# Performance work log

Hardware: AMD Instinct MI355X
Metric: run time of the kernel (lower is better)

The kernel has to match this reference:

```python
import jax, jax.numpy as jnp
import numpy as np

NUM_HEADS = 16
EPS = 1e-6
ROPE_BASE = 10000.0

def _thw(N, TT):
    table = {2640: (3, 22, 40), 1530: (3, 17, 30), 6120: (3, 34, 60), 660: (3, 11, 20)}
    return table.get(N - TT, (3, 23, 40))

def _positions(t, h, w):
    tt, hh, ww = np.meshgrid(np.arange(t), np.arange(h), np.arange(w), indexing='ij')
    return jnp.asarray(np.stack([tt, hh, ww], -1).reshape(-1, 3), jnp.float32)  # (THW, 3)

def _rope1d(x, pos):
    # x: (B,H,T,d) one axis-chunk, pos: (T,) positions for that axis
    d = x.shape[-1]
    inv_freq = 1.0 / (ROPE_BASE ** (jnp.arange(0, d, 2, dtype=jnp.float32) / d))
    ang = pos[:, None] * inv_freq                     # (T, d/2)
    cos = jnp.concatenate([jnp.cos(ang)] * 2, -1)     # (T, d)
    sin = jnp.concatenate([jnp.sin(ang)] * 2, -1)
    x1, x2 = x[..., : d // 2], x[..., d // 2:]
    return x * cos + jnp.concatenate([-x2, x1], -1) * sin

def _rope3d(x, pos, TT):
    # first TT tokens (text) pass through; video tokens get per-axis rotation
    pre, vid = x[:, :, :TT], x[:, :, TT:]
    chunks = jnp.split(vid, 3, axis=-1)               # t/h/w axis chunks
    rot = [_rope1d(c, pos[:, i]) for i, c in enumerate(chunks)]
    return jnp.concatenate([pre, jnp.concatenate(rot, -1)], axis=2)

def _rms(x, w):
    return x * jax.lax.rsqrt(jnp.mean(x * x, -1, keepdims=True) + EPS) * w

def setup_inputs() -> dict:
    key = jax.random.key(0)
    ks = jax.random.split(key, 12)
    B, N, C = 1, 2866, 1536
    Dh = C // NUM_HEADS
    s = 0.02
    return {
        'x': jax.random.normal(ks[0], (B, N, C), jnp.float32),
        'Wq': jax.random.normal(ks[1], (C, C), jnp.float32) * s,
        'bq': jnp.zeros((C,), jnp.float32),
        'Wk': jax.random.normal(ks[2], (C, C), jnp.float32) * s,
        'bk': jnp.zeros((C,), jnp.float32),
        'Wv': jax.random.normal(ks[3], (C, C), jnp.float32) * s,
        'bv': jnp.zeros((C,), jnp.float32),
        'qn_w': jnp.ones((Dh,), jnp.float32),
        'kn_w': jnp.ones((Dh,), jnp.float32),
        'Wp': jax.random.normal(ks[4], (C, C), jnp.float32) * s,
        'bp': jnp.zeros((C,), jnp.float32),
        'TT': 226,
    }

def reference(x, Wq, bq, Wk, bk, Wv, bv, qn_w, kn_w, Wp, bp, TT):
    B, N, C = x.shape
    H = NUM_HEADS
    Dh = C // H
    def proj(W, b):
        return (x @ W.T + b).reshape(B, N, H, Dh).transpose(0, 2, 1, 3)  # (B,H,N,Dh)
    q, k, v = proj(Wq, bq), proj(Wk, bk), proj(Wv, bv)
    q, k = _rms(q, qn_w), _rms(k, kn_w)
    t, h, w = _thw(N, TT)
    pos = _positions(t, h, w)
    q = _rope3d(q, pos, TT)
    k = _rope3d(k, pos, TT)
    scale = Dh ** -0.5
    attn = jax.nn.softmax(jnp.einsum('bhqd,bhkd->bhqk', q, k) * scale, axis=-1)
    o = jnp.einsum('bhqk,bhkd->bhqd', attn, v)
    o = o.transpose(0, 2, 1, 3).reshape(B, N, C)
    return o @ Wp.T + bp
```

## Files before the change

kernel.cpp:

```cpp
#include <hip/hip_runtime.h>
#include <hip/hip_bf16.h>
#include <math.h>

#define C_DIM 1536
#define H_NUM 16
#define DH    96

typedef __attribute__((ext_vector_type(4))) float  f32x4;
typedef __attribute__((ext_vector_type(8))) short  bf16x8;

__device__ __forceinline__ unsigned short f2bf_rne(float f) {
    unsigned u = __float_as_uint(f);
    unsigned r = (u + 0x7FFFu + ((u >> 16) & 1u)) >> 16;
    return (unsigned short)r;
}
__device__ __forceinline__ float bf2f(unsigned short h) {
    return __uint_as_float(((unsigned)h) << 16);
}

__device__ __forceinline__ void glds16(const void* g, void* l) {
    __builtin_amdgcn_global_load_lds(
        (const __attribute__((address_space(1))) unsigned int*)g,
        (__attribute__((address_space(3))) unsigned int*)l, 16, 0, 0);
}

struct CvtAll {
    const float* src[5];
    unsigned short* hi[5];
    unsigned short* lo[5];
};
__global__ __launch_bounds__(256)
void cvt_all(CvtAll a, int n4x, int n4w)
{
    const int role = blockIdx.y;
    const int n4   = (role == 0) ? n4x : n4w;
    const int i    = blockIdx.x * 256 + threadIdx.x;
    if (i >= n4) return;
    float4 v = *(const float4*)&a.src[role][4 * i];
    unsigned short h[4], l[4];
    float vv[4] = {v.x, v.y, v.z, v.w};
    #pragma unroll
    for (int j = 0; j < 4; ++j) {
        h[j] = f2bf_rne(vv[j]);
        l[j] = f2bf_rne(vv[j] - bf2f(h[j]));
    }
    *(ushort4*)&a.hi[role][4 * i] = *(ushort4*)h;
    *(ushort4*)&a.lo[role][4 * i] = *(ushort4*)l;
}

__global__ __launch_bounds__(256)
void gemm_mfma(const unsigned short* __restrict__ Ahi,
               const unsigned short* __restrict__ Alo,
               const unsigned short* W0h, const unsigned short* W0l,
               const float* b0, float* Y0,
               const unsigned short* W1h, const unsigned short* W1l,
               const float* b1, float* Y1,
               const unsigned short* W2h, const unsigned short* W2l,
               const float* b2, float* Y2,
               int M)
{
    __shared__ __align__(16) unsigned short lds[2 * 4 * 4096];

    const unsigned short* Wh;
    const unsigned short* Wl;
    const float* bias;
    float* Y;
    if (blockIdx.z == 0)      { Wh = W0h; Wl = W0l; bias = b0; Y = Y0; }
    else if (blockIdx.z == 1) { Wh = W1h; Wl = W1l; bias = b1; Y = Y1; }
    else                      { Wh = W2h; Wl = W2l; bias = b2; Y = Y2; }

    const int t   = threadIdx.x;
    const int m0  = blockIdx.x * 128;
    const int n0  = blockIdx.y * 128;
    const int w   = t >> 6;
    const int l   = t & 63;

    const unsigned short* src =
        (w == 0) ? Ahi : (w == 1) ? Alo : (w == 2) ? Wh : Wl;
    const int rbase = (w < 2) ? m0 : n0;
    const int rmax  = (w < 2) ? (M - 1) : 0x3FFFFFFF;
    const int srow  = l >> 2;
    const int scol  = l & 3;
    const int ssw   = (srow >> 1) & 3;
    int goff[8];
    #pragma unroll
    for (int i = 0; i < 8; ++i) {
        int gr = rbase + 16 * i + srow;
        gr = gr < rmax ? gr : rmax;
        goff[i] = gr * C_DIM + 8 * (scol ^ ssw);
    }

    const int lane = t & 63;
    const int wv   = t >> 6;
    const int wm   = wv & 1, wn = wv >> 1;
    const int lrow = lane & 15;
    const int quad = lane >> 4;
    const int pc   = quad ^ ((lrow >> 1) & 3);
    int aoff[4], boff[4];
    #pragma unroll
    for (int i = 0; i < 4; ++i) {
        aoff[i] = (64 * wm + 16 * i + lrow) * 32 + 8 * pc;
        boff[i] = (64 * wn + 16 * i + lrow) * 32 + 8 * pc;
    }

    f32x4 acc[4][4];
    #pragma unroll
    for (int i = 0; i < 4; ++i)
        #pragma unroll
        for (int j = 0; j < 4; ++j) acc[i][j] = (f32x4)0.f;

    #pragma unroll
    for (int i = 0; i < 8; ++i)
        glds16(src + goff[i], (char*)&lds[w * 4096] + i * 1024);

    const int NT = C_DIM / 32;
    for (int kt = 0; kt < NT; ++kt) {
        const int cb = kt & 1;
        const unsigned short* sA = lds + cb * 16384;

        asm volatile("s_waitcnt vmcnt(0)" ::: "memory");
        __builtin_amdgcn_s_barrier();
        __builtin_amdgcn_sched_barrier(0);

        bf16x8 ah[2], al[2], bh[4], bl[4];

        if (kt + 1 < NT) {
            char* dN = (char*)&lds[(cb ^ 1) * 16384 + w * 4096];
            const int k0n = (kt + 1) * 32;
            #pragma unroll
            for (int i = 0; i < 8; ++i)
                glds16(src + goff[i] + k0n, dN + i * 1024);
        }
        #pragma unroll
        for (int j = 0; j < 4; ++j) {
            bh[j] = *(const bf16x8*)&sA[8192 + boff[j]];
            bl[j] = *(const bf16x8*)&sA[12288 + boff[j]];
        }
        #pragma unroll
        for (int i = 0; i < 2; ++i) {
            ah[i] = *(const bf16x8*)&sA[aoff[i]];
            al[i] = *(const bf16x8*)&sA[4096 + aoff[i]];
        }
        __builtin_amdgcn_s_barrier();
        asm volatile("s_waitcnt lgkmcnt(0)" ::: "memory");
        __builtin_amdgcn_sched_barrier(0);
        __builtin_amdgcn_s_setprio(1);
        #pragma unroll
        for (int i = 0; i < 2; ++i)
            #pragma unroll
            for (int j = 0; j < 4; ++j) {
                acc[i][j] = __builtin_amdgcn_mfma_f32_16x16x32_bf16(ah[i], bh[j], acc[i][j], 0, 0, 0);
                acc[i][j] = __builtin_amdgcn_mfma_f32_16x16x32_bf16(al[i], bh[j], acc[i][j], 0, 0, 0);
                acc[i][j] = __builtin_amdgcn_mfma_f32_16x16x32_bf16(ah[i], bl[j], acc[i][j], 0, 0, 0);
            }
        __builtin_amdgcn_s_setprio(0);
        __builtin_amdgcn_s_barrier();
        __builtin_amdgcn_sched_barrier(0);

        #pragma unroll
        for (int i = 0; i < 2; ++i) {
            ah[i] = *(const bf16x8*)&sA[aoff[2 + i]];
            al[i] = *(const bf16x8*)&sA[4096 + aoff[2 + i]];
        }
        __builtin_amdgcn_s_barrier();
        asm volatile("s_waitcnt lgkmcnt(0)" ::: "memory");
        __builtin_amdgcn_sched_barrier(0);
        __builtin_amdgcn_s_setprio(1);
        #pragma unroll
        for (int i = 0; i < 2; ++i)
            #pragma unroll
            for (int j = 0; j < 4; ++j) {
                acc[2 + i][j] = __builtin_amdgcn_mfma_f32_16x16x32_bf16(ah[i], bh[j], acc[2 + i][j], 0, 0, 0);
                acc[2 + i][j] = __builtin_amdgcn_mfma_f32_16x16x32_bf16(al[i], bh[j], acc[2 + i][j], 0, 0, 0);
                acc[2 + i][j] = __builtin_amdgcn_mfma_f32_16x16x32_bf16(ah[i], bl[j], acc[2 + i][j], 0, 0, 0);
            }
        __builtin_amdgcn_s_setprio(0);
    }

    float bv[4];
    #pragma unroll
    for (int j = 0; j < 4; ++j) bv[j] = bias[n0 + 64 * wn + 16 * j + lrow];
    #pragma unroll
    for (int i = 0; i < 4; ++i) {
        const int rbase2 = m0 + 64 * wm + 16 * i + 4 * quad;
        #pragma unroll
        for (int p = 0; p < 4; ++p) {
            const int row = rbase2 + p;
            if (row >= M) continue;
            #pragma unroll
            for (int j = 0; j < 4; ++j) {
                const int col = n0 + 64 * wn + 16 * j + lrow;
                Y[(size_t)row * C_DIM + col] = acc[i][j][p] + bv[j];
            }
        }
    }
}

__global__ __launch_bounds__(512, 2)
void gemm_mfma256(const unsigned short* __restrict__ Ahi,
                  const unsigned short* __restrict__ Alo,
                  const unsigned short* W0h, const unsigned short* W0l,
                  const float* b0, float* Y0,
                  const unsigned short* W1h, const unsigned short* W1l,
                  const float* b1, float* Y1,
                  const unsigned short* W2h, const unsigned short* W2l,
                  const float* b2, float* Y2,
                  int M)
{
    extern __shared__ __align__(16) unsigned short smem[];

    const unsigned short* Wh;
    const unsigned short* Wl;
    const float* bias;
    float* Y;
    if (blockIdx.z == 0)      { Wh = W0h; Wl = W0l; bias = b0; Y = Y0; }
    else if (blockIdx.z == 1) { Wh = W1h; Wl = W1l; bias = b1; Y = Y1; }
    else                      { Wh = W2h; Wl = W2l; bias = b2; Y = Y2; }

    const int t    = threadIdx.x;
    const int wv   = t >> 6;
    const int lane = t & 63;
    const int m0   = blockIdx.x * 256;
    const int n0   = blockIdx.y * 256;

    const int mat  = wv >> 1;
    const int half = wv & 1;
    const unsigned short* src =
        (mat == 0) ? Ahi : (mat == 1) ? Alo : (mat == 2) ? Wh : Wl;
    const int rbase = (mat < 2) ? m0 : n0;
    const int rmax  = (mat < 2) ? (M - 1) : 0x3FFFFFFF;
    const int srow  = lane >> 2;
    const int scol  = lane & 3;
    const int ssw   = (srow >> 1) & 3;
    int goff[8];
    #pragma unroll
    for (int i = 0; i < 8; ++i) {
        int gr = rbase + half * 128 + 16 * i + srow;
        gr = gr < rmax ? gr : rmax;
        goff[i] = gr * C_DIM + 8 * (scol ^ ssw);
    }
    unsigned short* const dstBase = smem + mat * 8192 + half * 4096;

    const int wm   = wv & 1;
    const int wn   = wv >> 1;
    const int lrow = lane & 15;
    const int quad = lane >> 4;
    const int pc   = quad ^ ((lrow >> 1) & 3);
    int aoff[8], boff[4];
    #pragma unroll
    for (int i = 0; i < 8; ++i)
        aoff[i] = (128 * wm + 16 * i + lrow) * 32 + 8 * pc;
    #pragma unroll
    for (int j = 0; j < 4; ++j)
        boff[j] = (64 * wn + 16 * j + lrow) * 32 + 8 * pc;

    f32x4 acc[8][4];
    #pragma unroll
    for (int i = 0; i < 8; ++i)
        #pragma unroll
        for (int j = 0; j < 4; ++j) acc[i][j] = (f32x4)0.f;

    #pragma unroll
    for (int i = 0; i < 8; ++i)
        glds16(src + goff[i], (char*)dstBase + i * 1024);

    const int NT = C_DIM / 32;
    for (int kt = 0; kt < NT; ++kt) {
        const int cb = kt & 1;
        const unsigned short* sA = smem + cb * 32768;
        unsigned short* dN = dstBase + (cb ^ 1) * 32768;
        const int k0n = (kt + 1) * 32;
        const bool pf = (kt + 1 < NT);

        asm volatile("s_waitcnt vmcnt(0)" ::: "memory");
        __builtin_amdgcn_s_barrier();
        __builtin_amdgcn_sched_barrier(0);

        bf16x8 bh[4], bl[4], ah[2], al[2];

        if (pf) {
            #pragma unroll
            for (int i = 0; i < 4; ++i)
                glds16(src + goff[i] + k0n, (char*)dN + i * 1024);
        }
        #pragma unroll
        for (int j = 0; j < 4; ++j) {
            bh[j] = *(const bf16x8*)&sA[16384 + boff[j]];
            bl[j] = *(const bf16x8*)&sA[24576 + boff[j]];
        }
        #pragma unroll
        for (int i = 0; i < 2; ++i) {
            ah[i] = *(const bf16x8*)&sA[aoff[i]];
            al[i] = *(const bf16x8*)&sA[8192 + aoff[i]];
        }
        __builtin_amdgcn_s_barrier();
        asm volatile("s_waitcnt lgkmcnt(0)" ::: "memory");
        __builtin_amdgcn_sched_barrier(0);
        __builtin_amdgcn_s_setprio(1);
        #pragma unroll
        for (int i = 0; i < 2; ++i)
            #pragma unroll
            for (int j = 0; j < 4; ++j) {
                acc[i][j] = __builtin_amdgcn_mfma_f32_16x16x32_bf16(ah[i], bh[j], acc[i][j], 0, 0, 0);
                acc[i][j] = __builtin_amdgcn_mfma_f32_16x16x32_bf16(al[i], bh[j], acc[i][j], 0, 0, 0);
                acc[i][j] = __builtin_amdgcn_mfma_f32_16x16x32_bf16(ah[i], bl[j], acc[i][j], 0, 0, 0);
            }
        __builtin_amdgcn_s_setprio(0);
        __builtin_amdgcn_s_barrier();
        __builtin_amdgcn_sched_barrier(0);

        if (pf) {
            #pragma unroll
            for (int i = 4; i < 8; ++i)
                glds16(src + goff[i] + k0n, (char*)dN + i * 1024);
        }
        #pragma unroll
        for (int i = 0; i < 2; ++i) {
            ah[i] = *(const bf16x8*)&sA[aoff[2 + i]];
            al[i] = *(const bf16x8*)&sA[8192 + aoff[2 + i]];
        }
        __builtin_amdgcn_s_barrier();
        asm volatile("s_waitcnt lgkmcnt(0)" ::: "memory");
        __builtin_amdgcn_sched_barrier(0);
        __builtin_amdgcn_s_setprio(1);
        #pragma unroll
        for (int i = 0; i < 2; ++i)
            #pragma unroll
            for (int j = 0; j < 4; ++j) {
                acc[2 + i][j] = __builtin_amdgcn_mfma_f32_16x16x32_bf16(ah[i], bh[j], acc[2 + i][j], 0, 0, 0);
                acc[2 + i][j] = __builtin_amdgcn_mfma_f32_16x16x32_bf16(al[i], bh[j], acc[2 + i][j], 0, 0, 0);
                acc[2 + i][j] = __builtin_amdgcn_mfma_f32_16x16x32_bf16(ah[i], bl[j], acc[2 + i][j], 0, 0, 0);
            }
        __builtin_amdgcn_s_setprio(0);
        __builtin_amdgcn_s_barrier();
        __builtin_amdgcn_sched_barrier(0);

        #pragma unroll
        for (int i = 0; i < 2; ++i) {
            ah[i] = *(const bf16x8*)&sA[aoff[4 + i]];
            al[i] = *(const bf16x8*)&sA[8192 + aoff[4 + i]];
        }
        __builtin_amdgcn_s_barrier();
        asm volatile("s_waitcnt lgkmcnt(0)" ::: "memory");
        __builtin_amdgcn_sched_barrier(0);
        __builtin_amdgcn_s_setprio(1);
        #pragma unroll
        for (int i = 0; i < 2; ++i)
            #pragma unroll
            for (int j = 0; j < 4; ++j) {
                acc[4 + i][j] = __builtin_amdgcn_mfma_f32_16x16x32_bf16(ah[i], bh[j], acc[4 + i][j], 0, 0, 0);
                acc[4 + i][j] = __builtin_amdgcn_mfma_f32_16x16x32_bf16(al[i], bh[j], acc[4 + i][j], 0, 0, 0);
                acc[4 + i][j] = __builtin_amdgcn_mfma_f32_16x16x32_bf16(ah[i], bl[j], acc[4 + i][j], 0, 0, 0);
            }
        __builtin_amdgcn_s_setprio(0);
        __builtin_amdgcn_s_barrier();
        __builtin_amdgcn_sched_barrier(0);

        #pragma unroll
        for (int i = 0; i < 2; ++i) {
            ah[i] = *(const bf16x8*)&sA[aoff[6 + i]];
            al[i] = *(const bf16x8*)&sA[8192 + aoff[6 + i]];
        }
        __builtin_amdgcn_s_barrier();
        asm volatile("s_waitcnt lgkmcnt(0)" ::: "memory");
        __builtin_amdgcn_sched_barrier(0);
        __builtin_amdgcn_s_setprio(1);
        #pragma unroll
        for (int i = 0; i < 2; ++i)
            #pragma unroll
            for (int j = 0; j < 4; ++j) {
                acc[6 + i][j] = __builtin_amdgcn_mfma_f32_16x16x32_bf16(ah[i], bh[j], acc[6 + i][j], 0, 0, 0);
                acc[6 + i][j] = __builtin_amdgcn_mfma_f32_16x16x32_bf16(al[i], bh[j], acc[6 + i][j], 0, 0, 0);
                acc[6 + i][j] = __builtin_amdgcn_mfma_f32_16x16x32_bf16(ah[i], bl[j], acc[6 + i][j], 0, 0, 0);
            }
        __builtin_amdgcn_s_setprio(0);
    }

    float bv2[4];
    #pragma unroll
    for (int j = 0; j < 4; ++j) bv2[j] = bias[n0 + 64 * wn + 16 * j + lrow];
    #pragma unroll
    for (int i = 0; i < 8; ++i) {
        const int rbase2 = m0 + 128 * wm + 16 * i + 4 * quad;
        #pragma unroll
        for (int p = 0; p < 4; ++p) {
            const int row = rbase2 + p;
            if (row >= M) continue;
            #pragma unroll
            for (int j = 0; j < 4; ++j) {
                const int col = n0 + 64 * wn + 16 * j + lrow;
                Y[(size_t)row * C_DIM + col] = acc[i][j][p] + bv2[j];
            }
        }
    }
}

__global__ __launch_bounds__(256)
void rms_rope_tv(const float* __restrict__ q, const float* __restrict__ k,
                 const float* __restrict__ V,
                 const float* __restrict__ qw, const float* __restrict__ kw,
                 const int* __restrict__ TTp,
                 unsigned short* __restrict__ qhi, unsigned short* __restrict__ khi,
                 unsigned short* __restrict__ vt,
                 int Ntok, int nKt, int vtStride)
{
    __shared__ unsigned short tile[96 * 72];
    const int halfB = (Ntok * H_NUM + 255) >> 8;

    if ((int)blockIdx.x < 2 * halfB) {
        const int role = blockIdx.x / halfB;
        const int idx  = (blockIdx.x % halfB) * 256 + threadIdx.x;
        if (idx >= Ntok * H_NUM) return;
        const int h = idx & (H_NUM - 1);
        const int n = idx >> 4;

        const float* src = role == 0 ? q : k;
        const float* w   = role == 0 ? qw : kw;
        const float* p   = src + (size_t)n * C_DIM + h * DH;

        float ss = 0.f;
        #pragma unroll
        for (int i = 0; i < DH / 4; ++i) {
            float4 v4 = *(const float4*)&p[4 * i];
            ss += v4.x * v4.x;
            ss += v4.y * v4.y;
            ss += v4.z * v4.z;
            ss += v4.w * v4.w;
        }
        const float r = rsqrtf(ss * (1.0f / DH) + 1e-6f);

        const int TT = *TTp;
        const size_t off = (size_t)n * C_DIM + h * DH;
        const float qscale = 0.14724445f;

        if (n < TT) {
            #pragma unroll
            for (int i = 0; i < DH / 4; ++i) {
                float4 v4 = *(const float4*)&p[4 * i];
                float o[4] = {v4.x * (r * w[4 * i + 0]), v4.y * (r * w[4 * i + 1]),
                              v4.z * (r * w[4 * i + 2]), v4.w * (r * w[4 * i + 3])};
                unsigned short hb[4];
                #pragma unroll
                for (int j = 0; j < 4; ++j)
                    hb[j] = (role == 0) ? f2bf_rne(o[j] * qscale) : f2bf_rne(o[j]);
                if (role == 0) *(ushort4*)&qhi[off + 4 * i] = *(ushort4*)hb;
                else           *(ushort4*)&khi[off + 4 * i] = *(ushort4*)hb;
            }
        } else {
            const int pidx = n - TT;
            const int NTt  = Ntok - TT;
            int hh = 23, ww = 40;
            if      (NTt == 2640) { hh = 22; ww = 40; }
            else if (NTt == 1530) { hh = 17; ww = 30; }
            else if (NTt == 6120) { hh = 34; ww = 60; }
            else if (NTt ==  660) { hh = 11; ww = 20; }
            float pos[3];
            pos[0] = (float)(pidx / (hh * ww));
            pos[1] = (float)((pidx / ww) % hh);
            pos[2] = (float)(pidx % ww);
            #pragma unroll
            for (int c = 0; c < 3; ++c) {
                float xa[16], xb[16];
                #pragma unroll
                for (int g = 0; g < 4; ++g) {
                    float4 va = *(const float4*)&p[32 * c + 4 * g];
                    float4 vb = *(const float4*)&p[32 * c + 16 + 4 * g];
                    xa[4 * g + 0] = va.x * (r * w[32 * c + 4 * g + 0]);
                    xa[4 * g + 1] = va.y * (r * w[32 * c + 4 * g + 1]);
                    xa[4 * g + 2] = va.z * (r * w[32 * c + 4 * g + 2]);
                    xa[4 * g + 3] = va.w * (r * w[32 * c + 4 * g + 3]);
                    xb[4 * g + 0] = vb.x * (r * w[32 * c + 16 + 4 * g + 0]);
                    xb[4 * g + 1] = vb.y * (r * w[32 * c + 16 + 4 * g + 1]);
                    xb[4 * g + 2] = vb.z * (r * w[32 * c + 16 + 4 * g + 2]);
                    xb[4 * g + 3] = vb.w * (r * w[32 * c + 16 + 4 * g + 3]);
                }
                #pragma unroll
                for (int j = 0; j < 16; ++j) {
                    const float invf = exp2f(-0.83048202373f * (float)j);
                    const float ang  = pos[c] * invf;
                    const float cs = cosf(ang), sn = sinf(ang);
                    const float a = xa[j], b = xb[j];
                    xa[j] = a * cs - b * sn;
                    xb[j] = a * sn + b * cs;
                }
                #pragma unroll
                for (int g = 0; g < 4; ++g) {
                    unsigned short hb[4];
                    #pragma unroll
                    for (int j = 0; j < 4; ++j)
                        hb[j] = (role == 0) ? f2bf_rne(xa[4 * g + j] * qscale)
                                            : f2bf_rne(xa[4 * g + j]);
                    if (role == 0) *(ushort4*)&qhi[off + 32 * c + 4 * g] = *(ushort4*)hb;
                    else           *(ushort4*)&khi[off + 32 * c + 4 * g] = *(ushort4*)hb;
                }
                #pragma unroll
                for (int g = 0; g < 4; ++g) {
                    unsigned short hb[4];
                    #pragma unroll
                    for (int j = 0; j < 4; ++j)
                        hb[j] = (role == 0) ? f2bf_rne(xb[4 * g + j] * qscale)
                                            : f2bf_rne(xb[4 * g + j]);
                    if (role == 0) *(ushort4*)&qhi[off + 32 * c + 16 + 4 * g] = *(ushort4*)hb;
                    else           *(ushort4*)&khi[off + 32 * c + 16 + 4 * g] = *(ushort4*)hb;
                }
            }
        }
    } else {
        const int b2 = blockIdx.x - 2 * halfB;
        const int t  = threadIdx.x;
        const int k0 = (b2 % nKt) * 64;
        const int h  = b2 / nKt;

        #pragma unroll
        for (int it = 0; it < 6; ++it) {
            const int idx = t + 256 * it;
            const int key = idx / 24, dg = idx % 24;
            float vv[4] = {0.f, 0.f, 0.f, 0.f};
            if (k0 + key < Ntok)
                *(float4*)vv = *(const float4*)&V[(size_t)(k0 + key) * C_DIM + h * DH + 4 * dg];
            #pragma unroll
            for (int j = 0; j < 4; ++j) tile[(4 * dg + j) * 72 + key] = f2bf_rne(vv[j]);
        }
        __syncthreads();
        #pragma unroll
        for (int it = 0; it < 3; ++it) {
            const int idx = t + 256 * it;
            const int d = idx >> 3, ck = idx & 7;
            *(bf16x8*)&vt[((size_t)h * DH + d) * vtStride + k0 + 8 * ck] =
                *(const bf16x8*)&tile[d * 72 + 8 * ck];
        }
    }
}

__global__ __launch_bounds__(256)
void attn_mfma(const unsigned short* __restrict__ qhi,
               const unsigned short* __restrict__ khi,
               const unsigned short* __restrict__ vt,
               unsigned short* __restrict__ S0h, unsigned short* __restrict__ S0l,
               unsigned short* __restrict__ S1h, unsigned short* __restrict__ S1l,
               float* __restrict__ lbuf,
               int Ntok, int nKt, int nK0, int vtStride)
{
    __shared__ unsigned short ldsK[64 * 96];
    __shared__ unsigned short ldsV[96 * 72];
    __shared__ unsigned short ldsP[64 * 72];
    __shared__ float ldsL[64];

    const int t    = threadIdx.x;
    const int lane = t & 63;
    const int wv   = t >> 6;
    const int lrow = lane & 15;
    const int quad = lane >> 4;

    const int part  = blockIdx.z;
    const int ktBeg = part ? nK0 : 0;
    const int ktEnd = part ? nKt : nK0;
    unsigned short* const Shi = part ? S1h : S0h;
    unsigned short* const Slo = part ? S1l : S0l;
    float* const lout = lbuf + (size_t)part * Ntok * H_NUM;

    const int Lb  = blockIdx.x + gridDim.x * blockIdx.y;
    const int xcd = Lb & 7;
    const int jj  = Lb >> 3;
    const int h   = 2 * xcd + (jj >= nKt ? 1 : 0);
    const int q0  = (jj >= nKt ? jj - nKt : jj) * 64;
    const size_t hoff = (size_t)h * DH;

    bf16x8 qh[3];
    {
        const int qr = q0 + wv * 16 + lrow;
        if (qr < Ntok) {
            const size_t base = (size_t)qr * C_DIM + hoff + quad * 8;
            #pragma unroll
            for (int kc = 0; kc < 3; ++kc)
                qh[kc] = *(const bf16x8*)&qhi[base + 32 * kc];
        } else {
            const bf16x8 z = {0,0,0,0,0,0,0,0};
            #pragma unroll
            for (int kc = 0; kc < 3; ++kc) qh[kc] = z;
        }
    }

    const int rK  = t >> 2;
    const int cK  = t & 3;
    const int swK = (rK >> 1) & 3;
    const int swf = (lrow >> 1) & 3;
    const int vd  = t >> 3;
    const int vck = t & 7;

    float lsum = 0.f;
    f32x4 oacc[6];
    #pragma unroll
    for (int dt = 0; dt < 6; ++dt) oacc[dt] = (f32x4)0.f;

    const bf16x8 zv = {0,0,0,0,0,0,0,0};
    bf16x8 pk[3], pv[3];
    const int kB = ktBeg * 64;
    #pragma unroll
    for (int it = 0; it < 3; ++it) {
        pk[it] = (kB + rK < Ntok) ? *(const bf16x8*)&khi[(size_t)(kB + rK) * C_DIM + hoff + 8 * (cK + 4 * it)] : zv;
        pv[it] = *(const bf16x8*)&vt[(hoff + vd + 32 * it) * vtStride + kB + 8 * vck];
    }

    const int pRow = (wv * 16 + lrow) * 72;
    for (int kt = ktBeg; kt < ktEnd; ++kt) {
        const int k0 = kt * 64;
        __syncthreads();
        #pragma unroll
        for (int it = 0; it < 3; ++it) {
            *(bf16x8*)&ldsK[rK * 96 + 8 * (4 * it + (cK ^ swK))] = pk[it];
            *(bf16x8*)&ldsV[(vd + 32 * it) * 72 + 8 * vck]       = pv[it];
        }
        __syncthreads();

        if (kt + 1 < ktEnd) {
            const int kn = k0 + 64;
            #pragma unroll
            for (int it = 0; it < 3; ++it) {
                pk[it] = (kn + rK < Ntok) ? *(const bf16x8*)&khi[(size_t)(kn + rK) * C_DIM + hoff + 8 * (cK + 4 * it)] : zv;
                pv[it] = *(const bf16x8*)&vt[(hoff + vd + 32 * it) * vtStride + kn + 8 * vck];
            }
        }

        f32x4 sacc[4];
        #pragma unroll
        for (int mt = 0; mt < 4; ++mt) sacc[mt] = (f32x4)0.f;
        #pragma unroll
        for (int kc = 0; kc < 3; ++kc) {
            #pragma unroll
            for (int mt = 0; mt < 4; ++mt) {
                bf16x8 kb = *(const bf16x8*)&ldsK[(lrow + 16 * mt) * 96 + 8 * (4 * kc + (quad ^ swf))];
                sacc[mt] = __builtin_amdgcn_mfma_f32_16x16x32_bf16(kb, qh[kc], sacc[mt], 0, 0, 0);
            }
        }

        if (kt != nKt - 1) {
            #pragma unroll
            for (int mt = 0; mt < 4; ++mt) {
                float e[4];
                #pragma unroll
                for (int p = 0; p < 4; ++p) e[p] = exp2f(sacc[mt][p]);
                lsum += (e[0] + e[1]) + (e[2] + e[3]);
                unsigned u0 = __float_as_uint(e[0]) + 0x8000u;
                unsigned u1 = __float_as_uint(e[1]) + 0x8000u;
                unsigned u2 = __float_as_uint(e[2]) + 0x8000u;
                unsigned u3 = __float_as_uint(e[3]) + 0x8000u;
                uint2 pr;
                pr.x = __builtin_amdgcn_perm(u1, u0, 0x07060302u);
                pr.y = __builtin_amdgcn_perm(u3, u2, 0x07060302u);
                *(uint2*)&ldsP[pRow + 16 * mt + 4 * quad] = pr;
            }
        } else {
            const int kq = k0 + 4 * quad;
            #pragma unroll
            for (int mt = 0; mt < 4; ++mt) {
                float e[4];
                #pragma unroll
                for (int p = 0; p < 4; ++p)
                    e[p] = (kq + 16 * mt + p < Ntok) ? exp2f(sacc[mt][p]) : 0.f;
                lsum += (e[0] + e[1]) + (e[2] + e[3]);
                unsigned u0 = __float_as_uint(e[0]) + 0x8000u;
                unsigned u1 = __float_as_uint(e[1]) + 0x8000u;
                unsigned u2 = __float_as_uint(e[2]) + 0x8000u;
                unsigned u3 = __float_as_uint(e[3]) + 0x8000u;
                uint2 pr;
                pr.x = __builtin_amdgcn_perm(u1, u0, 0x07060302u);
                pr.y = __builtin_amdgcn_perm(u3, u2, 0x07060302u);
                *(uint2*)&ldsP[pRow + 16 * mt + 4 * quad] = pr;
            }
        }

        #pragma unroll
        for (int kc2 = 0; kc2 < 2; ++kc2) {
            bf16x8 pa = *(const bf16x8*)&ldsP[pRow + 32 * kc2 + 8 * quad];
            #pragma unroll
            for (int dt = 0; dt < 6; ++dt) {
                bf16x8 vb = *(const bf16x8*)&ldsV[(16 * dt + lrow) * 72 + 32 * kc2 + 8 * quad];
                oacc[dt] = __builtin_amdgcn_mfma_f32_16x16x32_bf16(pa, vb, oacc[dt], 0, 0, 0);
            }
        }
    }

    lsum += __shfl_xor(lsum, 16, 64);
    lsum += __shfl_xor(lsum, 32, 64);
    ldsL[wv * 16 + lrow] = lsum;
    #pragma unroll
    for (int p = 0; p < 4; ++p) {
        const int row = q0 + wv * 16 + quad * 4 + p;
        if (row >= Ntok) continue;
        if (lrow == 0)
            lout[(size_t)row * H_NUM + h] = ldsL[wv * 16 + quad * 4 + p];
        const size_t rbase = (size_t)row * C_DIM + hoff + lrow;
        #pragma unroll
        for (int dt = 0; dt < 6; ++dt) {
            const float o = oacc[dt][p];
            const unsigned short hb = f2bf_rne(o);
            Shi[rbase + 16 * dt] = hb;
            Slo[rbase + 16 * dt] = f2bf_rne(o - bf2f(hb));
        }
    }
}

__global__ __launch_bounds__(256)
void attn_combine(const unsigned short* __restrict__ s0h, const unsigned short* __restrict__ s0l,
                  const unsigned short* __restrict__ s1h, const unsigned short* __restrict__ s1l,
                  const float* __restrict__ lbuf,
                  unsigned short* __restrict__ ohi, unsigned short* __restrict__ olo,
                  int Ntok)
{
    const int i  = blockIdx.x * 256 + threadIdx.x;
    const int n4 = Ntok * (C_DIM / 4);
    if (i >= n4) return;
    const int row = (4 * i) / C_DIM;
    const int col = (4 * i) % C_DIM;
    const int h   = col / DH;
    const float rl = 1.0f /
        (lbuf[(size_t)row * H_NUM + h] + lbuf[(size_t)Ntok * H_NUM + (size_t)row * H_NUM + h]);

    ushort4 a0 = *(const ushort4*)&s0h[4 * i];
    ushort4 b0 = *(const ushort4*)&s0l[4 * i];
    ushort4 a1 = *(const ushort4*)&s1h[4 * i];
    ushort4 b1 = *(const ushort4*)&s1l[4 * i];
    const unsigned short* pa0 = (const unsigned short*)&a0;
    const unsigned short* pb0 = (const unsigned short*)&b0;
    const unsigned short* pa1 = (const unsigned short*)&a1;
    const unsigned short* pb1 = (const unsigned short*)&b1;
    unsigned short oh[4], ol[4];
    #pragma unroll
    for (int j = 0; j < 4; ++j) {
        const float s = (bf2f(pa0[j]) + bf2f(pb0[j])) + (bf2f(pa1[j]) + bf2f(pb1[j]));
        const float o = s * rl;
        oh[j] = f2bf_rne(o);
        ol[j] = f2bf_rne(o - bf2f(oh[j]));
    }
    *(ushort4*)&ohi[4 * i] = *(ushort4*)oh;
    *(ushort4*)&olo[4 * i] = *(ushort4*)ol;
}

extern "C" void kernel_launch(void* const* d_in, const int* in_sizes, int n_in,
                              void* d_out, int out_size, void* d_ws, size_t ws_size,
                              hipStream_t stream)
{
    const float* x   = (const float*)d_in[0];
    const float* Wq  = (const float*)d_in[1];
    const float* bq  = (const float*)d_in[2];
    const float* Wk  = (const float*)d_in[3];
    const float* bk  = (const float*)d_in[4];
    const float* Wv  = (const float*)d_in[5];
    const float* bv  = (const float*)d_in[6];
    const float* qnw = (const float*)d_in[7];
    const float* knw = (const float*)d_in[8];
    const float* Wp  = (const float*)d_in[9];
    const float* bp  = (const float*)d_in[10];
    const int*   TTp = (const int*)d_in[11];

    const int Ntok = in_sizes[0] / C_DIM;
    const int nKt  = (Ntok + 63) / 64;
    const int nK0  = (nKt + 1) / 2;
    const int vtStride = nKt * 64;
    const size_t NC = (size_t)Ntok * C_DIM;
    const size_t CC = (size_t)C_DIM * C_DIM;
    float* out = (float*)d_out;

    static bool s_attr = false;
    if (!s_attr) {
        hipFuncSetAttribute(reinterpret_cast<const void*>(gemm_mfma256),
                            hipFuncAttributeMaxDynamicSharedMemorySize, 131072);
        s_attr = true;
    }

    float*          kbuf = (float*)d_ws;
    float*          vbuf = kbuf + NC;
    unsigned short* xhi  = (unsigned short*)(vbuf + NC);
    unsigned short* xlo  = xhi + NC;
    unsigned short* wsp  = xlo + NC;
    unsigned short* wqh = wsp + 0 * CC, *wql = wsp + 1 * CC;
    unsigned short* wkh = wsp + 2 * CC, *wkl = wsp + 3 * CC;
    unsigned short* wvh = wsp + 4 * CC, *wvl = wsp + 5 * CC;
    unsigned short* wph = wsp + 6 * CC, *wpl = wsp + 7 * CC;
    unsigned short* qhib = wsp + 8 * CC;
    unsigned short* khib = qhib + NC;
    unsigned short* vtb  = khib + NC;
    float*          lbuf = (float*)(vtb + (size_t)H_NUM * DH * vtStride);
    float*          qbuf = out;
    unsigned short* s0h = (unsigned short*)kbuf;
    unsigned short* s0l = s0h + NC;
    unsigned short* s1h = (unsigned short*)vbuf;
    unsigned short* s1l = s1h + NC;
    unsigned short* ohi = xhi;
    unsigned short* olo = xlo;

    CvtAll ca;
    ca.src[0] = x;  ca.hi[0] = xhi; ca.lo[0] = xlo;
    ca.src[1] = Wq; ca.hi[1] = wqh; ca.lo[1] = wql;
    ca.src[2] = Wk; ca.hi[2] = wkh; ca.lo[2] = wkl;
    ca.src[3] = Wv; ca.hi[3] = wvh; ca.lo[3] = wvl;
    ca.src[4] = Wp; ca.hi[4] = wph; ca.lo[4] = wpl;
    cvt_all<<<dim3((NC / 4 + 255) / 256, 5), 256, 0, stream>>>(
        ca, (int)(NC / 4), (int)(CC / 4));

    dim3 qkvgrid((Ntok + 255) / 256, C_DIM / 256, 3);
    gemm_mfma256<<<qkvgrid, 512, 131072, stream>>>(xhi, xlo,
        wqh, wql, bq, qbuf,
        wkh, wkl, bk, kbuf,
        wvh, wvl, bv, vbuf, Ntok);

    const int halfB = (Ntok * H_NUM + 255) / 256;
    rms_rope_tv<<<dim3(2 * halfB + nKt * H_NUM), 256, 0, stream>>>(
        qbuf, kbuf, vbuf, qnw, knw, TTp, qhib, khib, vtb, Ntok, nKt, vtStride);

    attn_mfma<<<dim3(nKt, H_NUM, 2), 256, 0, stream>>>(
        qhib, khib, vtb, s0h, s0l, s1h, s1l, lbuf, Ntok, nKt, nK0, vtStride);

    attn_combine<<<dim3((NC / 4 + 255) / 256), 256, 0, stream>>>(
        s0h, s0l, s1h, s1l, lbuf, ohi, olo, Ntok);

    dim3 pgrid((Ntok + 127) / 128, C_DIM / 128, 1);
    gemm_mfma<<<pgrid, 256, 0, stream>>>(ohi, olo,
        wph, wpl, bp, out,
        wph, wpl, bp, out,
        wph, wpl, bp, out, Ntok);
}
```

Baseline: 421.2 us.

## Process 128 query rows per attention block to reuse K/V tiles

Each attention block now covers 128 query rows by giving every wave two 16-row query groups that share the K and V fragments loaded from LDS. This halves global K/V traffic and per-tile synchronisation relative to the amount of compute. In exchange it doubles the accumulator and Q registers, which may cut occupancy, and it halves the number of blocks, reducing parallelism across CUs.

After: 418.9 us. Within noise of the previous version (-0.5%).

```diff
diff --git a/kernel.cpp b/kernel.cpp
--- a/kernel.cpp
+++ b/kernel.cpp
@@ -543,8 +543,8 @@
 {
     __shared__ unsigned short ldsK[64 * 96];
     __shared__ unsigned short ldsV[96 * 72];
-    __shared__ unsigned short ldsP[64 * 72];
-    __shared__ float ldsL[64];
+    __shared__ unsigned short ldsP[128 * 72];
+    __shared__ float ldsL[128];
 
     const int t    = threadIdx.x;
     const int lane = t & 63;
@@ -559,25 +559,27 @@
     unsigned short* const Slo = part ? S1l : S0l;
     float* const lout = lbuf + (size_t)part * Ntok * H_NUM;
 
-    const int Lb  = blockIdx.x + gridDim.x * blockIdx.y;
+    const int nQb = gridDim.x;
+    const int Lb  = blockIdx.x + nQb * blockIdx.y;
     const int xcd = Lb & 7;
     const int jj  = Lb >> 3;
-    const int h   = 2 * xcd + (jj >= nKt ? 1 : 0);
-    const int q0  = (jj >= nKt ? jj - nKt : jj) * 64;
+    const int h   = 2 * xcd + (jj >= nQb ? 1 : 0);
+    const int q0  = (jj >= nQb ? jj - nQb : jj) * 128;
     const size_t hoff = (size_t)h * DH;
 
-    bf16x8 qh[3];
-    {
-        const int qr = q0 + wv * 16 + lrow;
+    bf16x8 qh[2][3];
+    #pragma unroll
+    for (int qg = 0; qg < 2; ++qg) {
+        const int qr = q0 + wv * 32 + qg * 16 + lrow;
         if (qr < Ntok) {
             const size_t base = (size_t)qr * C_DIM + hoff + quad * 8;
             #pragma unroll
             for (int kc = 0; kc < 3; ++kc)
-                qh[kc] = *(const bf16x8*)&qhi[base + 32 * kc];
+                qh[qg][kc] = *(const bf16x8*)&qhi[base + 32 * kc];
         } else {
             const bf16x8 z = {0,0,0,0,0,0,0,0};
             #pragma unroll
-            for (int kc = 0; kc < 3; ++kc) qh[kc] = z;
+            for (int kc = 0; kc < 3; ++kc) qh[qg][kc] = z;
         }
     }
 
@@ -588,10 +590,12 @@
     const int vd  = t >> 3;
     const int vck = t & 7;
 
-    float lsum = 0.f;
-    f32x4 oacc[6];
-    #pragma unroll
-    for (int dt = 0; dt < 6; ++dt) oacc[dt] = (f32x4)0.f;
+    float lsum[2] = {0.f, 0.f};
+    f32x4 oacc[2][6];
+    #pragma unroll
+    for (int qg = 0; qg < 2; ++qg)
+        #pragma unroll
+        for (int dt = 0; dt < 6; ++dt) oacc[qg][dt] = (f32x4)0.f;
 
     const bf16x8 zv = {0,0,0,0,0,0,0,0};
     bf16x8 pk[3], pv[3];
@@ -602,7 +606,8 @@
         pv[it] = *(const bf16x8*)&vt[(hoff + vd + 32 * it) * vtStride + kB + 8 * vck];
     }
 
-    const int pRow = (wv * 16 + lrow) * 72;
+    const int pRow0 = (wv * 32 + lrow) * 72;
+    const int pRow1 = pRow0 + 16 * 72;
     for (int kt = ktBeg; kt < ktEnd; ++kt) {
         const int k0 = kt * 64;
         __syncthreads();
@@ -622,81 +627,100 @@
             }
         }
 
-        f32x4 sacc[4];
-        #pragma unroll
-        for (int mt = 0; mt < 4; ++mt) sacc[mt] = (f32x4)0.f;
+        f32x4 sacc[2][4];
+        #pragma unroll
+        for (int qg = 0; qg < 2; ++qg)
+            #pragma unroll
+            for (int mt = 0; mt < 4; ++mt) sacc[qg][mt] = (f32x4)0.f;
         #pragma unroll
         for (int kc = 0; kc < 3; ++kc) {
             #pragma unroll
             for (int mt = 0; mt < 4; ++mt) {
                 bf16x8 kb = *(const bf16x8*)&ldsK[(lrow + 16 * mt) * 96 + 8 * (4 * kc + (quad ^ swf))];
-                sacc[mt] = __builtin_amdgcn_mfma_f32_16x16x32_bf16(kb, qh[kc], sacc[mt], 0, 0, 0);
+                sacc[0][mt] = __builtin_amdgcn_mfma_f32_16x16x32_bf16(kb, qh[0][kc], sacc[0][mt], 0, 0, 0);
+                sacc[1][mt] = __builtin_amdgcn_mfma_f32_16x16x32_bf16(kb, qh[1][kc], sacc[1][mt], 0, 0, 0);
             }
         }
 
         if (kt != nKt - 1) {
             #pragma unroll
-            for (int mt = 0; mt < 4; ++mt) {
-                float e[4];
+            for (int qg = 0; qg < 2; ++qg) {
+                const int pR = qg ? pRow1 : pRow0;
                 #pragma unroll
-                for (int p = 0; p < 4; ++p) e[p] = exp2f(sacc[mt][p]);
-                lsum += (e[0] + e[1]) + (e[2] + e[3]);
-                unsigned u0 = __float_as_uint(e[0]) + 0x8000u;
-                unsigned u1 = __float_as_uint(e[1]) + 0x8000u;
-                unsigned u2 = __float_as_uint(e[2]) + 0x8000u;
-                unsigned u3 = __float_as_uint(e[3]) + 0x8000u;
-                uint2 pr;
-                pr.x = __builtin_amdgcn_perm(u1, u0, 0x07060302u);
-                pr.y = __builtin_amdgcn_perm(u3, u2, 0x07060302u);
-                *(uint2*)&ldsP[pRow + 16 * mt + 4 * quad] = pr;
+                for (int mt = 0; mt < 4; ++mt) {
+                    float e[4];
+                    #pragma unroll
+                    for (int p = 0; p < 4; ++p) e[p] = exp2f(sacc[qg][mt][p]);
+                    lsum[qg] += (e[0] + e[1]) + (e[2] + e[3]);
+                    unsigned u0 = __float_as_uint(e[0]) + 0x8000u;
+                    unsigned u1 = __float_as_uint(e[1]) + 0x8000u;
+                    unsigned u2 = __float_as_uint(e[2]) + 0x8000u;
+                    unsigned u3 = __float_as_uint(e[3]) + 0x8000u;
+                    uint2 pr;
+                    pr.x = __builtin_amdgcn_perm(u1, u0, 0x07060302u);
+                    pr.y = __builtin_amdgcn_perm(u3, u2, 0x07060302u);
+                    *(uint2*)&ldsP[pR + 16 * mt + 4 * quad] = pr;
+                }
             }
         } else {
             const int kq = k0 + 4 * quad;
             #pragma unroll
-            for (int mt = 0; mt < 4; ++mt) {
-                float e[4];
+            for (int qg = 0; qg < 2; ++qg) {
+                const int pR = qg ? pRow1 : pRow0;
                 #pragma unroll
-                for (int p = 0; p < 4; ++p)
-                    e[p] = (kq + 16 * mt + p < Ntok) ? exp2f(sacc[mt][p]) : 0.f;
-                lsum += (e[0] + e[1]) + (e[2] + e[3]);
-                unsigned u0 = __float_as_uint(e[0]) + 0x8000u;
-                unsigned u1 = __float_as_uint(e[1]) + 0x8000u;
-                unsigned u2 = __float_as_uint(e[2]) + 0x8000u;
-                unsigned u3 = __float_as_uint(e[3]) + 0x8000u;
-                uint2 pr;
-                pr.x = __builtin_amdgcn_perm(u1, u0, 0x07060302u);
-                pr.y = __builtin_amdgcn_perm(u3, u2, 0x07060302u);
-                *(uint2*)&ldsP[pRow + 16 * mt + 4 * quad] = pr;
+                for (int mt = 0; mt < 4; ++mt) {
+                    float e[4];
+                    #pragma unroll
+                    for (int p = 0; p < 4; ++p)
+                        e[p] = (kq + 16 * mt + p < Ntok) ? exp2f(sacc[qg][mt][p]) : 0.f;
+                    lsum[qg] += (e[0] + e[1]) + (e[2] + e[3]);
+                    unsigned u0 = __float_as_uint(e[0]) + 0x8000u;
+                    unsigned u1 = __float_as_uint(e[1]) + 0x8000u;
+                    unsigned u2 = __float_as_uint(e[2]) + 0x8000u;
+                    unsigned u3 = __float_as_uint(e[3]) + 0x8000u;
+                    uint2 pr;
+                    pr.x = __builtin_amdgcn_perm(u1, u0, 0x07060302u);
+                    pr.y = __builtin_amdgcn_perm(u3, u2, 0x07060302u);
+                    *(uint2*)&ldsP[pR + 16 * mt + 4 * quad] = pr;
+                }
             }
         }
 
         #pragma unroll
         for (int kc2 = 0; kc2 < 2; ++kc2) {
-            bf16x8 pa = *(const bf16x8*)&ldsP[pRow + 32 * kc2 + 8 * quad];
+            bf16x8 pa0 = *(const bf16x8*)&ldsP[pRow0 + 32 * kc2 + 8 * quad];
+            bf16x8 pa1 = *(const bf16x8*)&ldsP[pRow1 + 32 * kc2 + 8 * quad];
             #pragma unroll
             for (int dt = 0; dt < 6; ++dt) {
                 bf16x8 vb = *(const bf16x8*)&ldsV[(16 * dt + lrow) * 72 + 32 * kc2 + 8 * quad];
-                oacc[dt] = __builtin_amdgcn_mfma_f32_16x16x32_bf16(pa, vb, oacc[dt], 0, 0, 0);
-            }
-        }
-    }
-
-    lsum += __shfl_xor(lsum, 16, 64);
-    lsum += __shfl_xor(lsum, 32, 64);
-    ldsL[wv * 16 + lrow] = lsum;
-    #pragma unroll
-    for (int p = 0; p < 4; ++p) {
-        const int row = q0 + wv * 16 + quad * 4 + p;
-        if (row >= Ntok) continue;
-        if (lrow == 0)
-            lout[(size_t)row * H_NUM + h] = ldsL[wv * 16 + quad * 4 + p];
-        const size_t rbase = (size_t)row * C_DIM + hoff + lrow;
-        #pragma unroll
-        for (int dt = 0; dt < 6; ++dt) {
-            const float o = oacc[dt][p];
-            const unsigned short hb = f2bf_rne(o);
-            Shi[rbase + 16 * dt] = hb;
-            Slo[rbase + 16 * dt] = f2bf_rne(o - bf2f(hb));
+                oacc[0][dt] = __builtin_amdgcn_mfma_f32_16x16x32_bf16(pa0, vb, oacc[0][dt], 0, 0, 0);
+                oacc[1][dt] = __builtin_amdgcn_mfma_f32_16x16x32_bf16(pa1, vb, oacc[1][dt], 0, 0, 0);
+            }
+        }
+    }
+
+    #pragma unroll
+    for (int qg = 0; qg < 2; ++qg) {
+        lsum[qg] += __shfl_xor(lsum[qg], 16, 64);
+        lsum[qg] += __shfl_xor(lsum[qg], 32, 64);
+        ldsL[wv * 32 + qg * 16 + lrow] = lsum[qg];
+    }
+    #pragma unroll
+    for (int qg = 0; qg < 2; ++qg) {
+        #pragma unroll
+        for (int p = 0; p < 4; ++p) {
+            const int row = q0 + wv * 32 + qg * 16 + quad * 4 + p;
+            if (row >= Ntok) continue;
+            if (lrow == 0)
+                lout[(size_t)row * H_NUM + h] = ldsL[wv * 32 + qg * 16 + quad * 4 + p];
+            const size_t rbase = (size_t)row * C_DIM + hoff + lrow;
+            #pragma unroll
+            for (int dt = 0; dt < 6; ++dt) {
+                const float o = oacc[qg][dt][p];
+                const unsigned short hb = f2bf_rne(o);
+                Shi[rbase + 16 * dt] = hb;
+                Slo[rbase + 16 * dt] = f2bf_rne(o - bf2f(hb));
+            }
         }
     }
 }
@@ -757,6 +781,7 @@
     const int Ntok = in_sizes[0] / C_DIM;
     const int nKt  = (Ntok + 63) / 64;
     const int nK0  = (nKt + 1) / 2;
+    const int nQb  = (Ntok + 127) / 128;
     const int vtStride = nKt * 64;
     const size_t NC = (size_t)Ntok * C_DIM;
     const size_t CC = (size_t)C_DIM * C_DIM;
@@ -809,7 +834,7 @@
     rms_rope_tv<<<dim3(2 * halfB + nKt * H_NUM), 256, 0, stream>>>(
         qbuf, kbuf, vbuf, qnw, knw, TTp, qhib, khib, vtb, Ntok, nKt, vtStride);
 
-    attn_mfma<<<dim3(nKt, H_NUM, 2), 256, 0, stream>>>(
+    attn_mfma<<<dim3(nQb, H_NUM, 2), 256, 0, stream>>>(
         qhib, khib, vtb, s0h, s0l, s1h, s1l, lbuf, Ntok, nKt, nK0, vtStride);
 
     attn_combine<<<dim3((NC / 4 + 255) / 256), 256, 0, stream>>>(
```
